# Performance work log

Hardware: AMD Instinct MI355X
Metric: run time of the kernel (lower is better)

## Reference

```python
import jax, jax.numpy as jnp
import numpy as np

# Constants matching init_kwargs
N_HEADS = 8
D_MODEL = 256
PATCH_NUM = 128
D_K = D_MODEL // N_HEADS  # 32
TEMP = 0.5
EPS = 1e-10


def setup_inputs() -> dict:
    key = jax.random.key(0)
    ks = jax.random.split(key, 20)
    s = 0.02
    d, h, n = D_MODEL, N_HEADS, PATCH_NUM
    inp = {
        "x": jax.random.normal(ks[0], (32, n, d), dtype=jnp.float32),
        "gumbel_u": jax.random.uniform(ks[1], (h, n, n, 2), dtype=jnp.float32),
        "memory_w": jax.random.normal(ks[2], (n, h * d), dtype=jnp.float32) * s,
        "fc_out_w": jax.random.normal(ks[3], (2 * d, d), dtype=jnp.float32) * s,
        "fc_out_b": jnp.zeros((d,), jnp.float32),
        "fc_cat_w": jax.random.normal(ks[4], (d, 2), dtype=jnp.float32) * s,
        "fc_cat_b": jnp.zeros((2,), jnp.float32),
        "wq": jax.random.normal(ks[5], (d, d), dtype=jnp.float32) * s,
        "bq": jnp.zeros((d,), jnp.float32),
        "wk": jax.random.normal(ks[6], (d, d), dtype=jnp.float32) * s,
        "bk": jnp.zeros((d,), jnp.float32),
        "wv": jax.random.normal(ks[7], (d, d), dtype=jnp.float32) * s,
        "bv": jnp.zeros((d,), jnp.float32),
        "out_w": jax.random.normal(ks[8], (d, d), dtype=jnp.float32) * s,
        "out_b": jnp.zeros((d,), jnp.float32),
        "mlp_w1": jax.random.normal(ks[9], (d, d), dtype=jnp.float32) * s,
        "mlp_b1": jnp.zeros((d,), jnp.float32),
        "mlp_w2": jax.random.normal(ks[10], (d, d), dtype=jnp.float32) * s,
        "mlp_b2": jnp.zeros((d,), jnp.float32),
    }
    return inp


def _forward(x, memory_w, fc_out_w, fc_out_b, fc_cat_w, fc_cat_b,
             wq, bq, wk, bk, wv, bv, out_w, out_b,
             mlp_w1, mlp_b1, mlp_w2, mlp_b2, gumbel_u):
    H, N, D = N_HEADS, PATCH_NUM, D_MODEL
    B = x.shape[0]

    # ---- SSConnectionLearning on memory feats ----
    # memory: Embedding(N, d_model*n_heads) -> feats [H, N, D]
    feats = memory_w.reshape(N, H, D).transpose(1, 0, 2)
    # rel_rec gathers row index i (receiver), rel_send gathers col index j (sender)
    senders = jnp.broadcast_to(feats[:, None, :, :], (H, N, N, D))   # feats[j]
    receivers = jnp.broadcast_to(feats[:, :, None, :], (H, N, N, D))  # feats[i]
    pair = jnp.concatenate([senders, receivers], axis=-1)  # [H,N,N,2D]
    hdn = jax.nn.relu(jnp.einsum('hijc,cd->hijd', pair, fc_out_w) + fc_out_b)
    logits = jnp.einsum('hijd,dk->hijk', hdn, fc_cat_w) + fc_cat_b  # [H,N,N,2]

    # gumbel-softmax, hard=True, straight-through
    g = -jnp.log(-jnp.log(gumbel_u + EPS) + EPS)
    y_soft = jax.nn.softmax((logits + g) / TEMP, axis=-1)
    y_hard = jax.nn.one_hot(jnp.argmax(y_soft, axis=-1), 2, dtype=y_soft.dtype)
    y = jax.lax.stop_gradient(y_hard - y_soft) + y_soft
    conn = y[..., 1]  # [H,N,N] learned sparse connection mask

    # ---- PatchIntegration (GELU MLP, dropout = identity in eval) ----
    xm = jax.nn.gelu(x @ mlp_w1 + mlp_b1)
    xm = xm @ mlp_w2 + mlp_b2

    # ---- Multihead attention masked by connection matrix ----
    q = (xm @ wq + bq).reshape(B, N, H, D_K).transpose(0, 2, 1, 3)  # [B,H,N,dk]
    k = (xm @ wk + bk).reshape(B, N, H, D_K).transpose(0, 2, 1, 3)
    v = (xm @ wv + bv).reshape(B, N, H, D_K).transpose(0, 2, 1, 3)
    scale = D_K ** -0.5
    scores = jnp.einsum('bhqd,bhkd->bhqk', q, k) * scale
    # additive mask: blocked where conn==0 (large negative keeps softmax finite)
    scores = scores + (conn[None] - 1.0) * 1e9
    attn = jax.nn.softmax(scores, axis=-1)
    out = jnp.einsum('bhqk,bhkd->bhqd', attn, v)
    out = out.transpose(0, 2, 1, 3).reshape(B, N, H * D_K)
    out = out @ out_w + out_b
    return out


def reference(x, gumbel_u, memory_w, fc_out_w, fc_out_b, fc_cat_w, fc_cat_b,
              wq, bq, wk, bk, wv, bv, out_w, out_b,
              mlp_w1, mlp_b1, mlp_w2, mlp_b2):
    return _forward(x, memory_w, fc_out_w, fc_out_b, fc_cat_w, fc_cat_b,
                    wq, bq, wk, bk, wv, bv, out_w, out_b,
                    mlp_w1, mlp_b1, mlp_w2, mlp_b2, gumbel_u)
```

## Files before the change

kernel.cpp:

```cpp
#include <hip/hip_runtime.h>
#include <hip/hip_bf16.h>
#include <math.h>


typedef short short8 __attribute__((ext_vector_type(8)));
typedef float f32x4 __attribute__((ext_vector_type(4)));

union V8 { uint4 u; short8 s; };

__device__ __forceinline__ float gelu_f(float x) {
    float inner = 0.7978845608028654f * (x + 0.044715f * x * x * x);
    return 0.5f * x * (1.0f + tanhf(inner));
}

__device__ __forceinline__ void split_bf16(float x, ushort& h, ushort& l) {
    __hip_bfloat16 bh = __float2bfloat16(x);
    float hf = __bfloat162float(bh);
    __hip_bfloat16 bl = __float2bfloat16(x - hf);
    h = __builtin_bit_cast(ushort, bh);
    l = __builtin_bit_cast(ushort, bl);
}

__device__ __forceinline__ ushort bf16bits(float x) {
    return __builtin_bit_cast(ushort, __float2bfloat16(x));
}
__device__ __forceinline__ float bits_to_f(ushort v) {
    return __builtin_bit_cast(float, ((uint)v) << 16);
}
__device__ __forceinline__ uint pk(float a, float b) {
    return (uint)bf16bits(a) | ((uint)bf16bits(b) << 16);
}
__device__ __forceinline__ short8 lds_frag(const ushort* p) {
    V8 v; v.u = *(const uint4*)p; return v.s;
}

__global__ __launch_bounds__(256) void k_wprep(
    const float* __restrict__ w0, const float* __restrict__ w1,
    const float* __restrict__ w2, const float* __restrict__ w3,
    const float* __restrict__ w4, const float* __restrict__ w5,
    const float* __restrict__ w6, const float* __restrict__ w7,
    ushort* __restrict__ hi, ushort* __restrict__ lo) {
    int m = blockIdx.x >> 4, tn = blockIdx.x & 15;
    const float* W = m == 0 ? w0 : m == 1 ? w1 : m == 2 ? w2 : m == 3 ? w3 :
                     m == 4 ? w4 : m == 5 ? w5 : m == 6 ? w6 : w7;
    ushort* Hm = hi + m * 65536;
    ushort* Lm = lo + m * 65536;
    int t = threadIdx.x;
    int n = tn * 16 + (t & 15);
    int k0 = (t >> 4) * 16;
    ushort hb[16], lb[16];
    #pragma unroll
    for (int kk = 0; kk < 16; ++kk)
        split_bf16(W[(k0 + kk) * 256 + n], hb[kk], lb[kk]);
    int ks = k0 >> 5;
    int q0 = (k0 >> 3) & 3;
    #pragma unroll
    for (int rb = 0; rb < 2; ++rb) {
        int lane = ((q0 + rb) << 4) | (t & 15);
        int idx = ((tn * 8 + ks) * 64 + lane) * 8;
        const ushort* hp = hb + rb * 8;
        const ushort* lp = lb + rb * 8;
        uint4 ph = { (uint)hp[0] | ((uint)hp[1] << 16), (uint)hp[2] | ((uint)hp[3] << 16),
                     (uint)hp[4] | ((uint)hp[5] << 16), (uint)hp[6] | ((uint)hp[7] << 16) };
        uint4 pl = { (uint)lp[0] | ((uint)lp[1] << 16), (uint)lp[2] | ((uint)lp[3] << 16),
                     (uint)lp[4] | ((uint)lp[5] << 16), (uint)lp[6] | ((uint)lp[7] << 16) };
        *(uint4*)(Hm + idx) = ph;
        *(uint4*)(Lm + idx) = pl;
    }
}

__global__ __launch_bounds__(256) void k_featproj(
    const float* __restrict__ memory_w,
    const ushort* __restrict__ Whi, const ushort* __restrict__ Wlo,
    float* __restrict__ A, float* __restrict__ Bm) {
    __shared__ __align__(16) ushort xhi[16 * 264], xlo[16 * 264];
    int t = threadIdx.x;
    int rt = blockIdx.x;
    int msel = blockIdx.y & 1, cq = blockIdx.y >> 1;
    #pragma unroll
    for (int ii = 0; ii < 4; ++ii) {
        int f4 = ii * 256 + t;
        int rr = f4 >> 6, c = (f4 & 63) * 4;
        int r = rt * 16 + rr;
        int h = r >> 7, n = r & 127;
        float4 xv = *(const float4*)(memory_w + n * 2048 + h * 256 + c);
        ushort hh[4], ll[4];
        split_bf16(xv.x, hh[0], ll[0]); split_bf16(xv.y, hh[1], ll[1]);
        split_bf16(xv.z, hh[2], ll[2]); split_bf16(xv.w, hh[3], ll[3]);
        uint2 ph = { (uint)hh[0] | ((uint)hh[1] << 16), (uint)hh[2] | ((uint)hh[3] << 16) };
        uint2 pl = { (uint)ll[0] | ((uint)ll[1] << 16), (uint)ll[2] | ((uint)ll[3] << 16) };
        *(uint2*)(xhi + rr * 264 + c) = ph;
        *(uint2*)(xlo + rr * 264 + c) = pl;
    }
    __syncthreads();
    int l = t & 63, w = t >> 6;
    int lr = l & 15, quad = l >> 4;
    int tg = cq * 4 + w;
    const uint4* H4 = (const uint4*)(Whi + (6 + msel) * 65536);
    const uint4* L4 = (const uint4*)(Wlo + (6 + msel) * 65536);
    const ushort* ah = xhi + lr * 264 + quad * 8;
    const ushort* al = xlo + lr * 264 + quad * 8;
    f32x4 acc = {};
    #pragma unroll 4
    for (int ks = 0; ks < 8; ++ks) {
        short8 a_h = lds_frag(ah + ks * 32);
        short8 a_l = lds_frag(al + ks * 32);
        int off = (tg * 8 + ks) * 64 + l;
        V8 bh, bl; bh.u = H4[off]; bl.u = L4[off];
        acc = __builtin_amdgcn_mfma_f32_16x16x32_bf16(a_h, bh.s, acc, 0, 0, 0);
        acc = __builtin_amdgcn_mfma_f32_16x16x32_bf16(a_l, bh.s, acc, 0, 0, 0);
        acc = __builtin_amdgcn_mfma_f32_16x16x32_bf16(a_h, bl.s, acc, 0, 0, 0);
    }
    float* O = msel ? Bm : A;
    int n0 = tg * 16 + lr;
    #pragma unroll
    for (int r = 0; r < 4; ++r)
        O[(rt * 16 + quad * 4 + r) * 256 + n0] = acc[r];
}

__global__ __launch_bounds__(256) void k_conn(
    const float* __restrict__ A, const float* __restrict__ Bm,
    const float* __restrict__ fc_out_b, const float* __restrict__ fc_cat_w,
    const float* __restrict__ fc_cat_b, const float* __restrict__ gumbel_u,
    ushort* __restrict__ maskb) {
    int blk = blockIdx.x;
    int h = blk >> 6, i0 = (blk & 63) * 2;
    int t = threadIdx.x;
    int j = t & 127, di = t >> 7;
    int i = i0 + di;
    __shared__ __align__(16) float sB[2 * 256];
    {
        float fb = fc_out_b[t];
        sB[t]       = Bm[(h * 128 + i0) * 256 + t] + fb;
        sB[256 + t] = Bm[(h * 128 + i0 + 1) * 256 + t] + fb;
    }
    __syncthreads();
    const float4* Arow4 = (const float4*)(A + (h * 128 + j) * 256);
    const float* sBr = sB + di * 256;
    float l0 = fc_cat_b[0], l1 = fc_cat_b[1];
    #pragma unroll 4
    for (int d4 = 0; d4 < 64; ++d4) {
        float4 av = Arow4[d4];
        int d = d4 * 4;
        float4 bv = *(const float4*)(sBr + d);
        float4 cwA = *(const float4*)(fc_cat_w + d * 2);
        float4 cwB = *(const float4*)(fc_cat_w + d * 2 + 4);
        float h0 = fmaxf(av.x + bv.x, 0.f);
        float h1 = fmaxf(av.y + bv.y, 0.f);
        float h2 = fmaxf(av.z + bv.z, 0.f);
        float h3 = fmaxf(av.w + bv.w, 0.f);
        l0 += h0 * cwA.x + h1 * cwA.z + h2 * cwB.x + h3 * cwB.z;
        l1 += h0 * cwA.y + h1 * cwA.w + h2 * cwB.y + h3 * cwB.w;
    }
    int gb = ((h * 128 + i) * 128 + j) * 2;
    float u0 = gumbel_u[gb], u1 = gumbel_u[gb + 1];
    float g0 = -logf(-logf(u0 + 1e-10f) + 1e-10f);
    float g1 = -logf(-logf(u1 + 1e-10f) + 1e-10f);
    bool on = (l1 + g1) > (l0 + g0);
    maskb[(h * 128 + i) * 128 + j] = bf16bits(on ? 0.f : -1e9f);
}

template <int ACT>
__global__ __launch_bounds__(256) void k_gemm16(
    const float* __restrict__ X, const ushort* __restrict__ Whi,
    const ushort* __restrict__ Wlo, const float* __restrict__ bias,
    float* __restrict__ Y) {
    __shared__ __align__(16) ushort xhi[16 * 264], xlo[16 * 264];
    int t = threadIdx.x;
    int r0 = blockIdx.x * 16;
    int ch = blockIdx.y;
    #pragma unroll
    for (int ii = 0; ii < 4; ++ii) {
        int f4 = ii * 256 + t;
        int row = f4 >> 6, c = (f4 & 63) * 4;
        float4 xv = *(const float4*)(X + (r0 + row) * 256 + c);
        ushort h[4], l[4];
        split_bf16(xv.x, h[0], l[0]); split_bf16(xv.y, h[1], l[1]);
        split_bf16(xv.z, h[2], l[2]); split_bf16(xv.w, h[3], l[3]);
        uint2 ph = { (uint)h[0] | ((uint)h[1] << 16), (uint)h[2] | ((uint)h[3] << 16) };
        uint2 pl = { (uint)l[0] | ((uint)l[1] << 16), (uint)l[2] | ((uint)l[3] << 16) };
        *(uint2*)(xhi + row * 264 + c) = ph;
        *(uint2*)(xlo + row * 264 + c) = pl;
    }
    __syncthreads();
    int l = t & 63, w = t >> 6;
    int lr = l & 15, quad = l >> 4;
    const ushort* ah = xhi + lr * 264 + quad * 8;
    const ushort* al = xlo + lr * 264 + quad * 8;
    const uint4* H4 = (const uint4*)Whi;
    const uint4* L4 = (const uint4*)Wlo;
    f32x4 acc[2] = {};
    #pragma unroll 2
    for (int ks = 0; ks < 8; ++ks) {
        short8 a_h = lds_frag(ah + ks * 32);
        short8 a_l = lds_frag(al + ks * 32);
        #pragma unroll
        for (int ti = 0; ti < 2; ++ti) {
            int tg = ch * 8 + w * 2 + ti;
            int off = (tg * 8 + ks) * 64 + l;
            V8 bh, bl; bh.u = H4[off]; bl.u = L4[off];
            acc[ti] = __builtin_amdgcn_mfma_f32_16x16x32_bf16(a_h, bh.s, acc[ti], 0, 0, 0);
            acc[ti] = __builtin_amdgcn_mfma_f32_16x16x32_bf16(a_l, bh.s, acc[ti], 0, 0, 0);
            acc[ti] = __builtin_amdgcn_mfma_f32_16x16x32_bf16(a_h, bl.s, acc[ti], 0, 0, 0);
        }
    }
    #pragma unroll
    for (int ti = 0; ti < 2; ++ti) {
        int n0 = (ch * 8 + w * 2 + ti) * 16 + lr;
        float bs = bias[n0];
        #pragma unroll
        for (int r = 0; r < 4; ++r) {
            float o = acc[ti][r] + bs;
            if (ACT) o = gelu_f(o);
            Y[(r0 + quad * 4 + r) * 256 + n0] = o;
        }
    }
}

__global__ __launch_bounds__(256) void k_qkv(
    const float* __restrict__ X, const ushort* __restrict__ Whi,
    const ushort* __restrict__ Wlo,
    const float* __restrict__ Bq, const float* __restrict__ Bk,
    const float* __restrict__ Bv,
    float* __restrict__ Q, float* __restrict__ K, float* __restrict__ V) {
    __shared__ __align__(16) ushort xhi[16 * 264], xlo[16 * 264];
    int t = threadIdx.x;
    int r0 = blockIdx.x * 16;
    int osel = blockIdx.y >> 1, ch = blockIdx.y & 1;
    #pragma unroll
    for (int ii = 0; ii < 4; ++ii) {
        int f4 = ii * 256 + t;
        int row = f4 >> 6, c = (f4 & 63) * 4;
        float4 xv = *(const float4*)(X + (r0 + row) * 256 + c);
        ushort h[4], l[4];
        split_bf16(xv.x, h[0], l[0]); split_bf16(xv.y, h[1], l[1]);
        split_bf16(xv.z, h[2], l[2]); split_bf16(xv.w, h[3], l[3]);
        uint2 ph = { (uint)h[0] | ((uint)h[1] << 16), (uint)h[2] | ((uint)h[3] << 16) };
        uint2 pl = { (uint)l[0] | ((uint)l[1] << 16), (uint)l[2] | ((uint)l[3] << 16) };
        *(uint2*)(xhi + row * 264 + c) = ph;
        *(uint2*)(xlo + row * 264 + c) = pl;
    }
    __syncthreads();
    int l = t & 63, w = t >> 6;
    int lr = l & 15, quad = l >> 4;
    const ushort* ah = xhi + lr * 264 + quad * 8;
    const ushort* al = xlo + lr * 264 + quad * 8;
    const uint4* H4 = (const uint4*)(Whi + (2 + osel) * 65536);
    const uint4* L4 = (const uint4*)(Wlo + (2 + osel) * 65536);
    f32x4 acc[2] = {};
    #pragma unroll 2
    for (int ks = 0; ks < 8; ++ks) {
        short8 a_h = lds_frag(ah + ks * 32);
        short8 a_l = lds_frag(al + ks * 32);
        #pragma unroll
        for (int ti = 0; ti < 2; ++ti) {
            int tg = ch * 8 + w * 2 + ti;
            int off = (tg * 8 + ks) * 64 + l;
            V8 bh, bl; bh.u = H4[off]; bl.u = L4[off];
            acc[ti] = __builtin_amdgcn_mfma_f32_16x16x32_bf16(a_h, bh.s, acc[ti], 0, 0, 0);
            acc[ti] = __builtin_amdgcn_mfma_f32_16x16x32_bf16(a_l, bh.s, acc[ti], 0, 0, 0);
            acc[ti] = __builtin_amdgcn_mfma_f32_16x16x32_bf16(a_h, bl.s, acc[ti], 0, 0, 0);
        }
    }
    const float* Bp = osel == 0 ? Bq : osel == 1 ? Bk : Bv;
    float* O = osel == 0 ? Q : osel == 1 ? K : V;
    #pragma unroll
    for (int ti = 0; ti < 2; ++ti) {
        int n0 = (ch * 8 + w * 2 + ti) * 16 + lr;
        float bs = Bp[n0];
        #pragma unroll
        for (int r = 0; r < 4; ++r)
            O[(r0 + quad * 4 + r) * 256 + n0] = acc[ti][r] + bs;
    }
}

__global__ __launch_bounds__(512) void k_attn_mfma(
    const float* __restrict__ Q, const float* __restrict__ K,
    const float* __restrict__ V, const ushort* __restrict__ maskb,
    float* __restrict__ AO) {
    int bh = blockIdx.x;
    int b = bh >> 3, h = bh & 7;
    int t = threadIdx.x;
    int lane = t & 63, w = t >> 6;
    __shared__ __align__(16) ushort vT[32 * 136];
    __shared__ __align__(16) ushort ps[128 * 136];
    #pragma unroll
    for (int it = 0; it < 2; ++it) {
        int f4 = it * 512 + t;
        int key = f4 >> 3, dq = (f4 & 7) * 4;
        float4 vv = *(const float4*)(V + b * 32768 + key * 256 + h * 32 + dq);
        vT[(dq + 0) * 136 + key] = bf16bits(vv.x);
        vT[(dq + 1) * 136 + key] = bf16bits(vv.y);
        vT[(dq + 2) * 136 + key] = bf16bits(vv.z);
        vT[(dq + 3) * 136 + key] = bf16bits(vv.w);
    }
    __syncthreads();
    int lr = lane & 15, quad = lane >> 4;
    const float* qp = Q + b * 32768 + (w * 16 + lr) * 256 + h * 32 + quad * 8;
    float4 q0 = *(const float4*)qp, q1 = *(const float4*)(qp + 4);
    V8 af;
    af.u.x = pk(q0.x, q0.y); af.u.y = pk(q0.z, q0.w);
    af.u.z = pk(q1.x, q1.y); af.u.w = pk(q1.z, q1.w);
    f32x4 s[8];
    #pragma unroll
    for (int ct = 0; ct < 8; ++ct) {
        const float* kp = K + b * 32768 + (ct * 16 + lr) * 256 + h * 32 + quad * 8;
        float4 k0 = *(const float4*)kp, k1 = *(const float4*)(kp + 4);
        V8 bf_;
        bf_.u.x = pk(k0.x, k0.y); bf_.u.y = pk(k0.z, k0.w);
        bf_.u.z = pk(k1.x, k1.y); bf_.u.w = pk(k1.z, k1.w);
        f32x4 z = {0.f, 0.f, 0.f, 0.f};
        s[ct] = __builtin_amdgcn_mfma_f32_16x16x32_bf16(af.s, bf_.s, z, 0, 0, 0);
    }
    const float scale = 0.17677669529663687f;
    const ushort* mrow = maskb + h * 16384;
    #pragma unroll
    for (int r = 0; r < 4; ++r) {
        int row = w * 16 + quad * 4 + r;
        float sv[8];
        float mx = -3.0e38f;
        #pragma unroll
        for (int ct = 0; ct < 8; ++ct) {
            float bias = bits_to_f(mrow[row * 128 + ct * 16 + lr]);
            sv[ct] = s[ct][r] * scale + bias;
            mx = fmaxf(mx, sv[ct]);
        }
        mx = fmaxf(mx, __shfl_xor(mx, 1));
        mx = fmaxf(mx, __shfl_xor(mx, 2));
        mx = fmaxf(mx, __shfl_xor(mx, 4));
        mx = fmaxf(mx, __shfl_xor(mx, 8));
        float sum = 0.f;
        #pragma unroll
        for (int ct = 0; ct < 8; ++ct) {
            sv[ct] = __expf(sv[ct] - mx);
            sum += sv[ct];
        }
        sum += __shfl_xor(sum, 1);
        sum += __shfl_xor(sum, 2);
        sum += __shfl_xor(sum, 4);
        sum += __shfl_xor(sum, 8);
        float iv = 1.f / sum;
        #pragma unroll
        for (int ct = 0; ct < 8; ++ct)
            ps[row * 136 + ct * 16 + lr] = bf16bits(sv[ct] * iv);
    }
    f32x4 o0 = {}, o1 = {};
    #pragma unroll
    for (int kk = 0; kk < 4; ++kk) {
        short8 pa = lds_frag(ps + (w * 16 + lr) * 136 + kk * 32 + quad * 8);
        short8 v0 = lds_frag(vT + lr * 136 + kk * 32 + quad * 8);
        short8 v1 = lds_frag(vT + (16 + lr) * 136 + kk * 32 + quad * 8);
        o0 = __builtin_amdgcn_mfma_f32_16x16x32_bf16(pa, v0, o0, 0, 0, 0);
        o1 = __builtin_amdgcn_mfma_f32_16x16x32_bf16(pa, v1, o1, 0, 0, 0);
    }
    #pragma unroll
    for (int r = 0; r < 4; ++r) {
        int row = w * 16 + quad * 4 + r;
        float* op = AO + b * 32768 + row * 256 + h * 32;
        op[lr] = o0[r];
        op[16 + lr] = o1[r];
    }
}

extern "C" void kernel_launch(void* const* d_in, const int* in_sizes, int n_in,
                              void* d_out, int out_size, void* d_ws, size_t ws_size,
                              hipStream_t stream) {
    const float* x        = (const float*)d_in[0];
    const float* gumbel_u = (const float*)d_in[1];
    const float* memory_w = (const float*)d_in[2];
    const float* fc_out_w = (const float*)d_in[3];
    const float* fc_out_b = (const float*)d_in[4];
    const float* fc_cat_w = (const float*)d_in[5];
    const float* fc_cat_b = (const float*)d_in[6];
    const float* wq       = (const float*)d_in[7];
    const float* bq       = (const float*)d_in[8];
    const float* wk       = (const float*)d_in[9];
    const float* bk       = (const float*)d_in[10];
    const float* wv_      = (const float*)d_in[11];
    const float* bv_      = (const float*)d_in[12];
    const float* out_w    = (const float*)d_in[13];
    const float* out_b    = (const float*)d_in[14];
    const float* mlp_w1   = (const float*)d_in[15];
    const float* mlp_b1   = (const float*)d_in[16];
    const float* mlp_w2   = (const float*)d_in[17];
    const float* mlp_b2   = (const float*)d_in[18];

    float* ws    = (float*)d_ws;
    float* A     = ws;
    float* Bm    = ws + 262144;
    ushort* mask = (ushort*)(ws + 524288);
    float* hbuf  = ws + 589824;
    float* xm    = ws + 1638400;
    float* q     = ws + 2686976;
    float* k     = ws + 3735552;
    float* v     = ws + 4784128;
    float* ao    = ws + 5832704;
    ushort* wf_hi = (ushort*)(ws + 6881280);
    ushort* wf_lo = wf_hi + 8 * 65536;
    float* out   = (float*)d_out;

    k_wprep<<<dim3(128), dim3(256), 0, stream>>>(
        mlp_w1, mlp_w2, wq, wk, wv_, out_w, fc_out_w, fc_out_w + 65536,
        wf_hi, wf_lo);
    k_featproj<<<dim3(64, 8), dim3(256), 0, stream>>>(memory_w, wf_hi, wf_lo, A, Bm);
    k_conn<<<dim3(512), dim3(256), 0, stream>>>(A, Bm, fc_out_b, fc_cat_w, fc_cat_b,
                                                gumbel_u, mask);
    k_gemm16<1><<<dim3(256, 2), dim3(256), 0, stream>>>(x, wf_hi + 0 * 65536,
                                                        wf_lo + 0 * 65536, mlp_b1, hbuf);
    k_gemm16<0><<<dim3(256, 2), dim3(256), 0, stream>>>(hbuf, wf_hi + 1 * 65536,
                                                        wf_lo + 1 * 65536, mlp_b2, xm);
    k_qkv<<<dim3(256, 6), dim3(256), 0, stream>>>(xm, wf_hi, wf_lo, bq, bk, bv_, q, k, v);
    k_attn_mfma<<<dim3(256), dim3(512), 0, stream>>>(q, k, v, mask, ao);
    k_gemm16<0><<<dim3(256, 2), dim3(256), 0, stream>>>(ao, wf_hi + 5 * 65536,
                                                        wf_lo + 5 * 65536, out_b, out);
}
```

Before: 170.0 us.

## Retile weight prep, connection, GEMM and attention kernels for more parallelism

```diff
diff --git a/kernel.cpp b/kernel.cpp
--- a/kernel.cpp
+++ b/kernel.cpp
@@ -40,30 +40,37 @@
     const float* __restrict__ w4, const float* __restrict__ w5,
     const float* __restrict__ w6, const float* __restrict__ w7,
     ushort* __restrict__ hi, ushort* __restrict__ lo) {
-    int m = blockIdx.x >> 4, tn = blockIdx.x & 15;
+    int bx = blockIdx.x;
+    int m = bx >> 4, ks = (bx >> 1) & 7, nh = bx & 1;
     const float* W = m == 0 ? w0 : m == 1 ? w1 : m == 2 ? w2 : m == 3 ? w3 :
                      m == 4 ? w4 : m == 5 ? w5 : m == 6 ? w6 : w7;
     ushort* Hm = hi + m * 65536;
     ushort* Lm = lo + m * 65536;
-    int t = threadIdx.x;
-    int n = tn * 16 + (t & 15);
-    int k0 = (t >> 4) * 16;
-    ushort hb[16], lb[16];
-    #pragma unroll
-    for (int kk = 0; kk < 16; ++kk)
-        split_bf16(W[(k0 + kk) * 256 + n], hb[kk], lb[kk]);
-    int ks = k0 >> 5;
-    int q0 = (k0 >> 3) & 3;
-    #pragma unroll
-    for (int rb = 0; rb < 2; ++rb) {
-        int lane = ((q0 + rb) << 4) | (t & 15);
-        int idx = ((tn * 8 + ks) * 64 + lane) * 8;
-        const ushort* hp = hb + rb * 8;
-        const ushort* lp = lb + rb * 8;
-        uint4 ph = { (uint)hp[0] | ((uint)hp[1] << 16), (uint)hp[2] | ((uint)hp[3] << 16),
-                     (uint)hp[4] | ((uint)hp[5] << 16), (uint)hp[6] | ((uint)hp[7] << 16) };
-        uint4 pl = { (uint)lp[0] | ((uint)lp[1] << 16), (uint)lp[2] | ((uint)lp[3] << 16),
-                     (uint)lp[4] | ((uint)lp[5] << 16), (uint)lp[6] | ((uint)lp[7] << 16) };
+    __shared__ __align__(16) float xs[32 * 132];
+    int t = threadIdx.x;
+    #pragma unroll
+    for (int p = 0; p < 4; ++p) {
+        int idx = p * 256 + t;
+        int row = idx >> 5, c4 = (idx & 31) * 4;
+        *(float4*)(xs + row * 132 + c4) =
+            *(const float4*)(W + (ks * 32 + row) * 256 + nh * 128 + c4);
+    }
+    __syncthreads();
+    int lane = t & 63, lr = lane & 15, quad = lane >> 4;
+    #pragma unroll
+    for (int it = 0; it < 2; ++it) {
+        int tgl = (t >> 6) + 4 * it;
+        int tg = nh * 8 + tgl;
+        int nl = tgl * 16 + lr;
+        ushort hb[8], lb[8];
+        #pragma unroll
+        for (int j = 0; j < 8; ++j)
+            split_bf16(xs[(quad * 8 + j) * 132 + nl], hb[j], lb[j]);
+        uint4 ph = { (uint)hb[0] | ((uint)hb[1] << 16), (uint)hb[2] | ((uint)hb[3] << 16),
+                     (uint)hb[4] | ((uint)hb[5] << 16), (uint)hb[6] | ((uint)hb[7] << 16) };
+        uint4 pl = { (uint)lb[0] | ((uint)lb[1] << 16), (uint)lb[2] | ((uint)lb[3] << 16),
+                     (uint)lb[4] | ((uint)lb[5] << 16), (uint)lb[6] | ((uint)lb[7] << 16) };
+        int idx = ((tg * 8 + ks) * 64 + lane) * 8;
         *(uint4*)(Hm + idx) = ph;
         *(uint4*)(Lm + idx) = pl;
     }
@@ -123,26 +130,32 @@
     const float* __restrict__ fc_out_b, const float* __restrict__ fc_cat_w,
     const float* __restrict__ fc_cat_b, const float* __restrict__ gumbel_u,
     ushort* __restrict__ maskb) {
-    int blk = blockIdx.x;
-    int h = blk >> 6, i0 = (blk & 63) * 2;
-    int t = threadIdx.x;
-    int j = t & 127, di = t >> 7;
-    int i = i0 + di;
-    __shared__ __align__(16) float sB[2 * 256];
-    {
-        float fb = fc_out_b[t];
-        sB[t]       = Bm[(h * 128 + i0) * 256 + t] + fb;
-        sB[256 + t] = Bm[(h * 128 + i0 + 1) * 256 + t] + fb;
-    }
-    __syncthreads();
-    const float4* Arow4 = (const float4*)(A + (h * 128 + j) * 256);
-    const float* sBr = sB + di * 256;
+    int bx = blockIdx.x;
+    int h = bx >> 6, it = (bx >> 3) & 7, jt = bx & 7;
+    int i0 = it * 16, j0 = jt * 16;
+    int t = threadIdx.x;
+    int il = t >> 4, jl = t & 15;
+    __shared__ __align__(16) float sA[16 * 260], sB[16 * 260];
+    #pragma unroll
+    for (int p = 0; p < 4; ++p) {
+        int idx = p * 256 + t;
+        int rr = idx >> 6, c = (idx & 63) * 4;
+        *(float4*)(sA + rr * 260 + c) =
+            *(const float4*)(A + (h * 128 + j0 + rr) * 256 + c);
+        float4 bv = *(const float4*)(Bm + (h * 128 + i0 + rr) * 256 + c);
+        float4 fb = *(const float4*)(fc_out_b + c);
+        bv.x += fb.x; bv.y += fb.y; bv.z += fb.z; bv.w += fb.w;
+        *(float4*)(sB + rr * 260 + c) = bv;
+    }
+    __syncthreads();
+    const float* Ar = sA + jl * 260;
+    const float* Br = sB + il * 260;
     float l0 = fc_cat_b[0], l1 = fc_cat_b[1];
     #pragma unroll 4
     for (int d4 = 0; d4 < 64; ++d4) {
-        float4 av = Arow4[d4];
         int d = d4 * 4;
-        float4 bv = *(const float4*)(sBr + d);
+        float4 av = *(const float4*)(Ar + d);
+        float4 bv = *(const float4*)(Br + d);
         float4 cwA = *(const float4*)(fc_cat_w + d * 2);
         float4 cwB = *(const float4*)(fc_cat_w + d * 2 + 4);
         float h0 = fmaxf(av.x + bv.x, 0.f);
@@ -152,10 +165,10 @@
         l0 += h0 * cwA.x + h1 * cwA.z + h2 * cwB.x + h3 * cwB.z;
         l1 += h0 * cwA.y + h1 * cwA.w + h2 * cwB.y + h3 * cwB.w;
     }
-    int gb = ((h * 128 + i) * 128 + j) * 2;
-    float u0 = gumbel_u[gb], u1 = gumbel_u[gb + 1];
-    float g0 = -logf(-logf(u0 + 1e-10f) + 1e-10f);
-    float g1 = -logf(-logf(u1 + 1e-10f) + 1e-10f);
+    int i = i0 + il, j = j0 + jl;
+    float2 uu = *(const float2*)(gumbel_u + ((h * 128 + i) * 128 + j) * 2);
+    float g0 = -logf(-logf(uu.x + 1e-10f) + 1e-10f);
+    float g1 = -logf(-logf(uu.y + 1e-10f) + 1e-10f);
     bool on = (l1 + g1) > (l0 + g0);
     maskb[(h * 128 + i) * 128 + j] = bf16bits(on ? 0.f : -1e9f);
 }
@@ -168,7 +181,6 @@
     __shared__ __align__(16) ushort xhi[16 * 264], xlo[16 * 264];
     int t = threadIdx.x;
     int r0 = blockIdx.x * 16;
-    int ch = blockIdx.y;
     #pragma unroll
     for (int ii = 0; ii < 4; ++ii) {
         int f4 = ii * 256 + t;
@@ -185,35 +197,29 @@
     __syncthreads();
     int l = t & 63, w = t >> 6;
     int lr = l & 15, quad = l >> 4;
+    int tg = blockIdx.y * 4 + w;
     const ushort* ah = xhi + lr * 264 + quad * 8;
     const ushort* al = xlo + lr * 264 + quad * 8;
     const uint4* H4 = (const uint4*)Whi;
     const uint4* L4 = (const uint4*)Wlo;
-    f32x4 acc[2] = {};
-    #pragma unroll 2
+    f32x4 acc = {};
+    #pragma unroll 4
     for (int ks = 0; ks < 8; ++ks) {
         short8 a_h = lds_frag(ah + ks * 32);
         short8 a_l = lds_frag(al + ks * 32);
-        #pragma unroll
-        for (int ti = 0; ti < 2; ++ti) {
-            int tg = ch * 8 + w * 2 + ti;
-            int off = (tg * 8 + ks) * 64 + l;
-            V8 bh, bl; bh.u = H4[off]; bl.u = L4[off];
-            acc[ti] = __builtin_amdgcn_mfma_f32_16x16x32_bf16(a_h, bh.s, acc[ti], 0, 0, 0);
-            acc[ti] = __builtin_amdgcn_mfma_f32_16x16x32_bf16(a_l, bh.s, acc[ti], 0, 0, 0);
-            acc[ti] = __builtin_amdgcn_mfma_f32_16x16x32_bf16(a_h, bl.s, acc[ti], 0, 0, 0);
-        }
-    }
-    #pragma unroll
-    for (int ti = 0; ti < 2; ++ti) {
-        int n0 = (ch * 8 + w * 2 + ti) * 16 + lr;
-        float bs = bias[n0];
-        #pragma unroll
-        for (int r = 0; r < 4; ++r) {
-            float o = acc[ti][r] + bs;
-            if (ACT) o = gelu_f(o);
-            Y[(r0 + quad * 4 + r) * 256 + n0] = o;
-        }
+        int off = (tg * 8 + ks) * 64 + l;
+        V8 bh, bl; bh.u = H4[off]; bl.u = L4[off];
+        acc = __builtin_amdgcn_mfma_f32_16x16x32_bf16(a_h, bh.s, acc, 0, 0, 0);
+        acc = __builtin_amdgcn_mfma_f32_16x16x32_bf16(a_l, bh.s, acc, 0, 0, 0);
+        acc = __builtin_amdgcn_mfma_f32_16x16x32_bf16(a_h, bl.s, acc, 0, 0, 0);
+    }
+    int n0 = tg * 16 + lr;
+    float bs = bias[n0];
+    #pragma unroll
+    for (int r = 0; r < 4; ++r) {
+        float o = acc[r] + bs;
+        if (ACT) o = gelu_f(o);
+        Y[(r0 + quad * 4 + r) * 256 + n0] = o;
     }
 }
 
@@ -226,7 +232,7 @@
     __shared__ __align__(16) ushort xhi[16 * 264], xlo[16 * 264];
     int t = threadIdx.x;
     int r0 = blockIdx.x * 16;
-    int osel = blockIdx.y >> 1, ch = blockIdx.y & 1;
+    int osel = blockIdx.y >> 2, cq = blockIdx.y & 3;
     #pragma unroll
     for (int ii = 0; ii < 4; ++ii) {
         int f4 = ii * 256 + t;
@@ -243,50 +249,44 @@
     __syncthreads();
     int l = t & 63, w = t >> 6;
     int lr = l & 15, quad = l >> 4;
+    int tg = cq * 4 + w;
     const ushort* ah = xhi + lr * 264 + quad * 8;
     const ushort* al = xlo + lr * 264 + quad * 8;
     const uint4* H4 = (const uint4*)(Whi + (2 + osel) * 65536);
     const uint4* L4 = (const uint4*)(Wlo + (2 + osel) * 65536);
-    f32x4 acc[2] = {};
-    #pragma unroll 2
+    f32x4 acc = {};
+    #pragma unroll 4
     for (int ks = 0; ks < 8; ++ks) {
         short8 a_h = lds_frag(ah + ks * 32);
         short8 a_l = lds_frag(al + ks * 32);
-        #pragma unroll
-        for (int ti = 0; ti < 2; ++ti) {
-            int tg = ch * 8 + w * 2 + ti;
-            int off = (tg * 8 + ks) * 64 + l;
-            V8 bh, bl; bh.u = H4[off]; bl.u = L4[off];
-            acc[ti] = __builtin_amdgcn_mfma_f32_16x16x32_bf16(a_h, bh.s, acc[ti], 0, 0, 0);
-            acc[ti] = __builtin_amdgcn_mfma_f32_16x16x32_bf16(a_l, bh.s, acc[ti], 0, 0, 0);
-            acc[ti] = __builtin_amdgcn_mfma_f32_16x16x32_bf16(a_h, bl.s, acc[ti], 0, 0, 0);
-        }
+        int off = (tg * 8 + ks) * 64 + l;
+        V8 bh, bl; bh.u = H4[off]; bl.u = L4[off];
+        acc = __builtin_amdgcn_mfma_f32_16x16x32_bf16(a_h, bh.s, acc, 0, 0, 0);
+        acc = __builtin_amdgcn_mfma_f32_16x16x32_bf16(a_l, bh.s, acc, 0, 0, 0);
+        acc = __builtin_amdgcn_mfma_f32_16x16x32_bf16(a_h, bl.s, acc, 0, 0, 0);
     }
     const float* Bp = osel == 0 ? Bq : osel == 1 ? Bk : Bv;
     float* O = osel == 0 ? Q : osel == 1 ? K : V;
-    #pragma unroll
-    for (int ti = 0; ti < 2; ++ti) {
-        int n0 = (ch * 8 + w * 2 + ti) * 16 + lr;
-        float bs = Bp[n0];
-        #pragma unroll
-        for (int r = 0; r < 4; ++r)
-            O[(r0 + quad * 4 + r) * 256 + n0] = acc[ti][r] + bs;
-    }
-}
-
-__global__ __launch_bounds__(512) void k_attn_mfma(
+    int n0 = tg * 16 + lr;
+    float bs = Bp[n0];
+    #pragma unroll
+    for (int r = 0; r < 4; ++r)
+        O[(r0 + quad * 4 + r) * 256 + n0] = acc[r] + bs;
+}
+
+__global__ __launch_bounds__(256) void k_attn_mfma(
     const float* __restrict__ Q, const float* __restrict__ K,
     const float* __restrict__ V, const ushort* __restrict__ maskb,
     float* __restrict__ AO) {
-    int bh = blockIdx.x;
-    int b = bh >> 3, h = bh & 7;
+    int bx = blockIdx.x;
+    int b = bx >> 4, h = (bx >> 1) & 7, rh = bx & 1;
     int t = threadIdx.x;
     int lane = t & 63, w = t >> 6;
     __shared__ __align__(16) ushort vT[32 * 136];
-    __shared__ __align__(16) ushort ps[128 * 136];
-    #pragma unroll
-    for (int it = 0; it < 2; ++it) {
-        int f4 = it * 512 + t;
+    __shared__ __align__(16) ushort ps[64 * 136];
+    #pragma unroll
+    for (int it = 0; it < 4; ++it) {
+        int f4 = it * 256 + t;
         int key = f4 >> 3, dq = (f4 & 7) * 4;
         float4 vv = *(const float4*)(V + b * 32768 + key * 256 + h * 32 + dq);
         vT[(dq + 0) * 136 + key] = bf16bits(vv.x);
@@ -296,7 +296,8 @@
     }
     __syncthreads();
     int lr = lane & 15, quad = lane >> 4;
-    const float* qp = Q + b * 32768 + (w * 16 + lr) * 256 + h * 32 + quad * 8;
+    int rt = rh * 4 + w;
+    const float* qp = Q + b * 32768 + (rt * 16 + lr) * 256 + h * 32 + quad * 8;
     float4 q0 = *(const float4*)qp, q1 = *(const float4*)(qp + 4);
     V8 af;
     af.u.x = pk(q0.x, q0.y); af.u.y = pk(q0.z, q0.w);
@@ -316,12 +317,13 @@
     const ushort* mrow = maskb + h * 16384;
     #pragma unroll
     for (int r = 0; r < 4; ++r) {
-        int row = w * 16 + quad * 4 + r;
+        int lrow = w * 16 + quad * 4 + r;
+        int grow = rt * 16 + quad * 4 + r;
         float sv[8];
         float mx = -3.0e38f;
         #pragma unroll
         for (int ct = 0; ct < 8; ++ct) {
-            float bias = bits_to_f(mrow[row * 128 + ct * 16 + lr]);
+            float bias = bits_to_f(mrow[grow * 128 + ct * 16 + lr]);
             sv[ct] = s[ct][r] * scale + bias;
             mx = fmaxf(mx, sv[ct]);
         }
@@ -342,7 +344,7 @@
         float iv = 1.f / sum;
         #pragma unroll
         for (int ct = 0; ct < 8; ++ct)
-            ps[row * 136 + ct * 16 + lr] = bf16bits(sv[ct] * iv);
+            ps[lrow * 136 + ct * 16 + lr] = bf16bits(sv[ct] * iv);
     }
     f32x4 o0 = {}, o1 = {};
     #pragma unroll
@@ -355,8 +357,8 @@
     }
     #pragma unroll
     for (int r = 0; r < 4; ++r) {
-        int row = w * 16 + quad * 4 + r;
-        float* op = AO + b * 32768 + row * 256 + h * 32;
+        int grow = rt * 16 + quad * 4 + r;
+        float* op = AO + b * 32768 + grow * 256 + h * 32;
         op[lr] = o0[r];
         op[16 + lr] = o1[r];
     }
@@ -405,12 +407,12 @@
     k_featproj<<<dim3(64, 8), dim3(256), 0, stream>>>(memory_w, wf_hi, wf_lo, A, Bm);
     k_conn<<<dim3(512), dim3(256), 0, stream>>>(A, Bm, fc_out_b, fc_cat_w, fc_cat_b,
                                                 gumbel_u, mask);
-    k_gemm16<1><<<dim3(256, 2), dim3(256), 0, stream>>>(x, wf_hi + 0 * 65536,
+    k_gemm16<1><<<dim3(256, 4), dim3(256), 0, stream>>>(x, wf_hi + 0 * 65536,
                                                         wf_lo + 0 * 65536, mlp_b1, hbuf);
-    k_gemm16<0><<<dim3(256, 2), dim3(256), 0, stream>>>(hbuf, wf_hi + 1 * 65536,
+    k_gemm16<0><<<dim3(256, 4), dim3(256), 0, stream>>>(hbuf, wf_hi + 1 * 65536,
                                                         wf_lo + 1 * 65536, mlp_b2, xm);
-    k_qkv<<<dim3(256, 6), dim3(256), 0, stream>>>(xm, wf_hi, wf_lo, bq, bk, bv_, q, k, v);
-    k_attn_mfma<<<dim3(256), dim3(512), 0, stream>>>(q, k, v, mask, ao);
-    k_gemm16<0><<<dim3(256, 2), dim3(256), 0, stream>>>(ao, wf_hi + 5 * 65536,
+    k_qkv<<<dim3(256, 12), dim3(256), 0, stream>>>(xm, wf_hi, wf_lo, bq, bk, bv_, q, k, v);
+    k_attn_mfma<<<dim3(512), dim3(256), 0, stream>>>(q, k, v, mask, ao);
+    k_gemm16<0><<<dim3(256, 4), dim3(256), 0, stream>>>(ao, wf_hi + 5 * 65536,
                                                         wf_lo + 5 * 65536, out_b, out);
 }
```

After: 161.4 us. -5.0%, faster.
